# Kernel tuning notes

Hardware: AMD Instinct MI355X
Metric: run time of the kernel (lower is better)

## Reference

```python
import jax, jax.numpy as jnp
import numpy as np

N_EMBD = 2048
N_HEAD = 16
HEAD_SIZE = N_EMBD // N_HEAD


def setup_inputs() -> dict:
    key = jax.random.key(0)
    k1, k2, k3 = jax.random.split(key, 3)
    x = jax.random.normal(k1, (4, 2048, N_EMBD), dtype=jnp.float32)
    # Linear weights stored as (in, out) for x @ W
    scale = 1.0 / np.sqrt(N_EMBD)
    w_qkv = jax.random.normal(k2, (N_EMBD, 3 * N_EMBD), dtype=jnp.float32) * scale
    w_proj = jax.random.normal(k3, (N_EMBD, N_EMBD), dtype=jnp.float32) * scale
    return {"x": x, "w_qkv": w_qkv, "w_proj": w_proj}


def reference(x, w_qkv, w_proj):
    B, T, C = x.shape
    qkv = x @ w_qkv  # [B, T, 3C]
    q, k, v = jnp.split(qkv, 3, axis=-1)
    # [B, H, T, Dh]
    def heads(t):
        return t.reshape(B, T, N_HEAD, HEAD_SIZE).transpose(0, 2, 1, 3)
    q, k, v = heads(q), heads(k), heads(v)
    scores = jnp.einsum('bhqd,bhkd->bhqk', q, k) * (1.0 / np.sqrt(HEAD_SIZE))
    causal = jnp.tril(jnp.ones((T, T), dtype=bool))
    scores = jnp.where(causal, scores, jnp.finfo(scores.dtype).min)
    att = jax.nn.softmax(scores, axis=-1)
    y = jnp.einsum('bhqk,bhkd->bhqd', att, v)
    y = y.transpose(0, 2, 1, 3).reshape(B, T, C)
    return y @ w_proj
```

## Files before the change

kernel.cpp:

```cpp
#include <hip/hip_runtime.h>

typedef unsigned short u16;
typedef unsigned int u32;
typedef __bf16 bf16x8 __attribute__((ext_vector_type(8)));
typedef float f32x4 __attribute__((ext_vector_type(4)));

__device__ __forceinline__ u16 f2bf(float f) {
  u32 u = __builtin_bit_cast(u32, f);
  return (u16)((u + 0x7fffu + ((u >> 16) & 1u)) >> 16);
}

__device__ __forceinline__ f32x4 mfma16(bf16x8 a, bf16x8 b, f32x4 c) {
  return __builtin_amdgcn_mfma_f32_16x16x32_bf16(a, b, c, 0, 0, 0);
}

struct alignas(8) U16x4 { u16 x, y, z, w; };

#define AS1 __attribute__((address_space(1)))
#define AS3 __attribute__((address_space(3)))
__device__ __forceinline__ void gl16(const u16* g, u16* l) {
  __builtin_amdgcn_global_load_lds((const AS1 u32*)g, (AS3 u32*)l, 16, 0, 0);
}

__global__ __launch_bounds__(256) void k_f32_to_bf16(const float* __restrict__ in,
                                                     u16* __restrict__ out, long n4) {
  long i = (long)blockIdx.x * blockDim.x + threadIdx.x;
  long stride = (long)gridDim.x * blockDim.x;
  for (; i < n4; i += stride) {
    float4 v = ((const float4*)in)[i];
    U16x4 o{f2bf(v.x), f2bf(v.y), f2bf(v.z), f2bf(v.w)};
    ((U16x4*)out)[i] = o;
  }
}

__global__ __launch_bounds__(256) void k_transpose_f32_to_bf16(const float* __restrict__ in,
                                                               u16* __restrict__ out,
                                                               int rows, int cols) {
  __shared__ float tile[32][33];
  int bc = blockIdx.x * 32, br = blockIdx.y * 32;
  int tx = threadIdx.x, ty = threadIdx.y;
  for (int i = 0; i < 32; i += 8)
    tile[ty + i][tx] = in[(long)(br + ty + i) * cols + bc + tx];
  __syncthreads();
  for (int i = 0; i < 32; i += 8)
    out[(long)(bc + ty + i) * rows + br + tx] = f2bf(tile[tx][ty + i]);
}

__global__ __launch_bounds__(256) void k_transpose_v(const u16* __restrict__ qkv,
                                                     u16* __restrict__ vt) {
  __shared__ u16 tile[32][33];
  int bh = blockIdx.z; int b = bh >> 4, h = bh & 15;
  int t0 = blockIdx.y * 32, d0 = blockIdx.x * 32;
  int tx = threadIdx.x, ty = threadIdx.y;
  const u16* src = qkv + (long)(b * 2048) * 6144 + 4096 + h * 128;
  for (int i = 0; i < 32; i += 8)
    tile[ty + i][tx] = src[(long)(t0 + ty + i) * 6144 + d0 + tx];
  __syncthreads();
  u16* dst = vt + (long)bh * 128 * 2048;
  for (int i = 0; i < 32; i += 8)
    dst[(long)(d0 + ty + i) * 2048 + t0 + tx] = tile[tx][ty + i];
}

template <typename OutT>
__global__ __launch_bounds__(512, 2) void k_gemm256(const u16* __restrict__ A,
                                                    const u16* __restrict__ Bt,
                                                    OutT* __restrict__ C,
                                                    int M, int N, int K) {
  __shared__ alignas(16) u16 As[4][8192];
  __shared__ alignas(16) u16 Bs[4][8192];

  int gx = gridDim.x;
  int nwg = gx * gridDim.y;
  int bid = blockIdx.y * gx + blockIdx.x;
  int swz = (bid & 7) * (nwg >> 3) + (bid >> 3);
  int rem = swz % (gx * 4);
  int bx = rem >> 2;
  int by = (swz / (gx * 4)) * 4 + (rem & 3);

  int tid = threadIdx.x;
  int lane = tid & 63;
  int w = tid >> 6;
  int wr = w >> 2, wc = w & 3;
  int lr = lane & 15, lg = lane >> 4;
  long brow = (long)by * 256, bcol = (long)bx * 256;

  int rS[2], cS[2];
#pragma unroll
  for (int i = 0; i < 2; ++i) {
    int q = i * 512 + tid;
    rS[i] = q >> 2;
    cS[i] = ((q & 3) ^ ((rS[i] >> 1) & 3)) << 3;
  }
  const u16* Ab = A + brow * K;
  const u16* Bb = Bt + bcol * K;

  int offA[8], offB[4];
#pragma unroll
  for (int m = 0; m < 8; ++m) {
    int row = wr * 128 + m * 16 + lr;
    offA[m] = row * 32 + ((lg ^ ((row >> 1) & 3)) << 3);
  }
#pragma unroll
  for (int n = 0; n < 4; ++n) {
    int row = wc * 64 + n * 16 + lr;
    offB[n] = row * 32 + ((lg ^ ((row >> 1) & 3)) << 3);
  }

  f32x4 zero = {0.f, 0.f, 0.f, 0.f};
  f32x4 acc[8][4];
#pragma unroll
  for (int m = 0; m < 8; ++m)
#pragma unroll
    for (int n = 0; n < 4; ++n) acc[m][n] = zero;

  int NS = K >> 5;

#define STAGE256(SBUF, KT)                                                          \
  do {                                                                              \
    int kk_ = (KT) << 5;                                                            \
    gl16(Ab + (long)rS[0] * K + kk_ + cS[0], &As[SBUF][(0 * 512 + w * 64) * 8]);    \
    gl16(Ab + (long)rS[1] * K + kk_ + cS[1], &As[SBUF][(1 * 512 + w * 64) * 8]);    \
    gl16(Bb + (long)rS[0] * K + kk_ + cS[0], &Bs[SBUF][(0 * 512 + w * 64) * 8]);    \
    gl16(Bb + (long)rS[1] * K + kk_ + cS[1], &Bs[SBUF][(1 * 512 + w * 64) * 8]);    \
  } while (0)

  STAGE256(0, 0);
  STAGE256(1, 1);
  STAGE256(2, 2);
  asm volatile("s_waitcnt vmcnt(8)" ::: "memory");
  __builtin_amdgcn_s_barrier();

  for (int s = 0; s < NS; ++s) {
    int cb = s & 3;
    bf16x8 af[8], bfn[4];
#pragma unroll
    for (int m = 0; m < 8; ++m) af[m] = *(const bf16x8*)&As[cb][offA[m]];
#pragma unroll
    for (int n = 0; n < 4; ++n) bfn[n] = *(const bf16x8*)&Bs[cb][offB[n]];
    int t = s + 3;
    int tb = t & 3;
    if (t > NS - 1) t = NS - 1;
    STAGE256(tb, t);
    __builtin_amdgcn_s_setprio(1);
#pragma unroll
    for (int m = 0; m < 4; ++m)
#pragma unroll
      for (int n = 0; n < 4; ++n) acc[m][n] = mfma16(af[m], bfn[n], acc[m][n]);
    __builtin_amdgcn_s_setprio(0);
    __builtin_amdgcn_s_setprio(1);
#pragma unroll
    for (int m = 4; m < 8; ++m)
#pragma unroll
      for (int n = 0; n < 4; ++n) acc[m][n] = mfma16(af[m], bfn[n], acc[m][n]);
    __builtin_amdgcn_s_setprio(0);
    asm volatile("s_waitcnt vmcnt(8)" ::: "memory");
    __builtin_amdgcn_s_barrier();
  }
#undef STAGE256
  asm volatile("s_waitcnt vmcnt(0)" ::: "memory");

#pragma unroll
  for (int m = 0; m < 8; ++m)
#pragma unroll
    for (int n = 0; n < 4; ++n)
#pragma unroll
      for (int r = 0; r < 4; ++r) {
        long row = brow + wr * 128 + m * 16 + lg * 4 + r;
        long col = bcol + wc * 64 + n * 16 + lr;
        float v = acc[m][n][r];
        if constexpr (sizeof(OutT) == 2)
          C[row * N + col] = (OutT)f2bf(v);
        else
          C[row * N + col] = v;
      }
}

__global__ __launch_bounds__(256, 2) void k_attn2(const u16* __restrict__ qkv,
                                                  const u16* __restrict__ vt,
                                                  u16* __restrict__ y) {
  __shared__ alignas(16) u16 Ks[2][64 * 128];
  __shared__ alignas(16) u16 Vs[2][128 * 64];
  __shared__ alignas(16) u16 Ps[4][32 * 64];

  int bh = blockIdx.x;
  int qb = 15 - (int)blockIdx.y;
  int b = bh >> 4, h = bh & 15;
  int tid = threadIdx.x;
  int lane = tid & 63;
  int w = tid >> 6;
  int lr = lane & 15, lg = lane >> 4;
  int x7 = lr & 7;
  const float scale = 0.08838834764831845f;

  const u16* kbase = qkv + (long)(b * 2048) * 6144 + 2048 + h * 128;
  const u16* vtbh = vt + (long)bh * 128 * 2048;
  int qbase = qb * 128 + w * 32;

  const u16* qptr = qkv + (long)(qb * 128 + b * 2048) * 6144 + h * 128;
  bf16x8 qf[2][4];
  for (int qsub = 0; qsub < 2; ++qsub)
    for (int dc = 0; dc < 4; ++dc)
      qf[qsub][dc] = *(const bf16x8*)(qptr + (long)(w * 32 + qsub * 16 + lr) * 6144 + dc * 32 + lg * 8);

  f32x4 zero = {0.f, 0.f, 0.f, 0.f};
  f32x4 o[2][8];
  for (int qs = 0; qs < 2; ++qs)
    for (int ds = 0; ds < 8; ++ds) o[qs][ds] = zero;
  float m_run[2] = {-1e30f, -1e30f};
  float l_run[2] = {0.f, 0.f};

  int nkt = 2 * qb + 2;
  int qmaxw = qbase + 31;
  u16* Pw = &Ps[w][0];

#define STAGE(BUF, KT)                                                          \
  do {                                                                          \
    for (int i_ = 0; i_ < 4; ++i_) {                                            \
      int rl_ = w * 16 + i_ * 4;                                                \
      int row_ = rl_ + (lane >> 4);                                             \
      int ch_ = (lane & 15) ^ (row_ & 7);                                       \
      gl16(kbase + (long)((KT)*64 + row_) * 6144 + ch_ * 8, &Ks[BUF][rl_ * 128]); \
    }                                                                           \
    for (int i_ = 0; i_ < 4; ++i_) {                                            \
      int dl_ = w * 32 + i_ * 8;                                                \
      int d_ = dl_ + (lane >> 3);                                               \
      int ch_ = (lane & 7) ^ (d_ & 7);                                          \
      gl16(vtbh + (long)d_ * 2048 + (KT)*64 + ch_ * 8, &Vs[BUF][dl_ * 64]);     \
    }                                                                           \
  } while (0)

#define COMPUTE(BUF, KT)                                                        \
  do {                                                                          \
    const u16* Kb = &Ks[BUF][0];                                                \
    const u16* Vb = &Vs[BUF][0];                                                \
    f32x4 s[2][4];                                                              \
    for (int qs = 0; qs < 2; ++qs)                                              \
      for (int ks = 0; ks < 4; ++ks) s[qs][ks] = zero;                          \
    for (int ks = 0; ks < 4; ++ks) {                                            \
      int row = ks * 16 + lr;                                                   \
      for (int dc = 0; dc < 4; ++dc) {                                          \
        bf16x8 kf = *(const bf16x8*)(Kb + row * 128 + ((dc * 4 + lg) ^ x7) * 8); \
        s[0][ks] = mfma16(kf, qf[0][dc], s[0][ks]);                             \
        s[1][ks] = mfma16(kf, qf[1][dc], s[1][ks]);                             \
      }                                                                         \
    }                                                                           \
    for (int qs = 0; qs < 2; ++qs) {                                            \
      int qg = qbase + qs * 16 + lr;                                            \
      float p[16];                                                              \
      float tmax = -1e30f;                                                      \
      for (int ks = 0; ks < 4; ++ks)                                            \
        for (int r = 0; r < 4; ++r) {                                           \
          int key = (KT)*64 + ks * 16 + lg * 4 + r;                             \
          float v = (key <= qg) ? s[qs][ks][r] * scale : -1e30f;                \
          p[ks * 4 + r] = v;                                                    \
          tmax = fmaxf(tmax, v);                                                \
        }                                                                       \
      tmax = fmaxf(tmax, __shfl_xor(tmax, 16));                                 \
      tmax = fmaxf(tmax, __shfl_xor(tmax, 32));                                 \
      float m_new = fmaxf(m_run[qs], tmax);                                     \
      float alpha = __expf(m_run[qs] - m_new);                                  \
      float psum = 0.f;                                                         \
      for (int i = 0; i < 16; ++i) {                                            \
        p[i] = __expf(p[i] - m_new);                                            \
        psum += p[i];                                                           \
      }                                                                         \
      psum += __shfl_xor(psum, 16);                                             \
      psum += __shfl_xor(psum, 32);                                             \
      l_run[qs] = l_run[qs] * alpha + psum;                                     \
      m_run[qs] = m_new;                                                        \
      int prow = qs * 16 + lr;                                                  \
      for (int ks = 0; ks < 4; ++ks) {                                          \
        U16x4 pk{f2bf(p[ks * 4 + 0]), f2bf(p[ks * 4 + 1]),                      \
                 f2bf(p[ks * 4 + 2]), f2bf(p[ks * 4 + 3])};                     \
        int chunk = ks * 2 + (lg >> 1);                                         \
        *(U16x4*)&Pw[prow * 64 + ((chunk ^ x7) * 8) + (lg & 1) * 4] = pk;       \
      }                                                                         \
      float alr[4];                                                             \
      for (int r = 0; r < 4; ++r) alr[r] = __shfl(alpha, lg * 4 + r);           \
      for (int ds = 0; ds < 8; ++ds)                                            \
        for (int r = 0; r < 4; ++r) o[qs][ds][r] *= alr[r];                     \
    }                                                                           \
    asm volatile("s_waitcnt lgkmcnt(0)" ::: "memory");                          \
    for (int j = 0; j < 2; ++j) {                                               \
      int chv = ((j * 4 + lg) ^ x7) * 8;                                        \
      bf16x8 pa0 = *(const bf16x8*)&Pw[(0 * 16 + lr) * 64 + chv];               \
      bf16x8 pa1 = *(const bf16x8*)&Pw[(1 * 16 + lr) * 64 + chv];               \
      for (int ds = 0; ds < 8; ++ds) {                                          \
        bf16x8 vf = *(const bf16x8*)(Vb + (ds * 16 + lr) * 64 + chv);           \
        o[0][ds] = mfma16(pa0, vf, o[0][ds]);                                   \
        o[1][ds] = mfma16(pa1, vf, o[1][ds]);                                   \
      }                                                                         \
    }                                                                           \
  } while (0)

  int buf = 0;
  STAGE(0, 0);
  asm volatile("s_waitcnt vmcnt(0)" ::: "memory");
  __builtin_amdgcn_s_barrier();
  for (int kt = 0; kt < nkt - 1; ++kt) {
    STAGE(buf ^ 1, kt + 1);
    if (kt * 64 <= qmaxw) COMPUTE(buf, kt);
    asm volatile("s_waitcnt vmcnt(0) lgkmcnt(0)" ::: "memory");
    __builtin_amdgcn_s_barrier();
    buf ^= 1;
  }
  {
    int kt = nkt - 1;
    if (kt * 64 <= qmaxw) COMPUTE(buf, kt);
  }
#undef STAGE
#undef COMPUTE

  float linv[2][4];
  for (int qs = 0; qs < 2; ++qs)
    for (int r = 0; r < 4; ++r) linv[qs][r] = 1.0f / __shfl(l_run[qs], lg * 4 + r);
  u16* yb = y + (long)(b * 2048 + qb * 128 + w * 32) * 2048 + h * 128;
  for (int qs = 0; qs < 2; ++qs)
    for (int ds = 0; ds < 8; ++ds)
      for (int r = 0; r < 4; ++r)
        yb[(long)(qs * 16 + lg * 4 + r) * 2048 + ds * 16 + lr] = f2bf(o[qs][ds][r] * linv[qs][r]);
}

extern "C" void kernel_launch(void* const* d_in, const int* in_sizes, int n_in,
                              void* d_out, int out_size, void* d_ws, size_t ws_size,
                              hipStream_t stream) {
  const float* x = (const float*)d_in[0];
  const float* w_qkv = (const float*)d_in[1];
  const float* w_proj = (const float*)d_in[2];
  float* out = (float*)d_out;

  char* ws = (char*)d_ws;
  if (ws_size < 201326592ull) return;
  u16* QKV = (u16*)(ws);
  u16* WqT = (u16*)(ws + 100663296);
  u16* WpT = (u16*)(ws + 125829120);
  u16* Xb  = (u16*)(ws + 134217728);
  u16* Vt  = (u16*)(ws + 167772160);

  dim3 tb32x8(32, 8);

  k_f32_to_bf16<<<2048, 256, 0, stream>>>(x, Xb, (8192L * 2048) / 4);
  k_transpose_f32_to_bf16<<<dim3(192, 64), tb32x8, 0, stream>>>(w_qkv, WqT, 2048, 6144);
  k_transpose_f32_to_bf16<<<dim3(64, 64), tb32x8, 0, stream>>>(w_proj, WpT, 2048, 2048);

  k_gemm256<u16><<<dim3(24, 32), 512, 0, stream>>>(Xb, WqT, QKV, 8192, 6144, 2048);

  k_transpose_v<<<dim3(4, 64, 64), tb32x8, 0, stream>>>(QKV, Vt);

  k_attn2<<<dim3(64, 16), 256, 0, stream>>>(QKV, Vt, Xb );

  k_gemm256<float><<<dim3(8, 32), 512, 0, stream>>>(Xb, WpT, out, 8192, 2048, 2048);
}
```

Baseline: 416.9 us.

## Widen attention blocks to 256 queries with triple-buffered K/V pipeline

```diff
diff --git a/kernel.cpp b/kernel.cpp
--- a/kernel.cpp
+++ b/kernel.cpp
@@ -175,15 +175,16 @@
       }
 }
 
-__global__ __launch_bounds__(256, 2) void k_attn2(const u16* __restrict__ qkv,
+__global__ __launch_bounds__(512, 1) void k_attn3(const u16* __restrict__ qkv,
                                                   const u16* __restrict__ vt,
                                                   u16* __restrict__ y) {
-  __shared__ alignas(16) u16 Ks[2][64 * 128];
-  __shared__ alignas(16) u16 Vs[2][128 * 64];
-  __shared__ alignas(16) u16 Ps[4][32 * 64];
+  __shared__ alignas(16) u16 Ks[3][64 * 128];
+  __shared__ alignas(16) u16 Vs[3][128 * 64];
+  __shared__ alignas(16) u16 Ps[8][32 * 64];
 
   int bh = blockIdx.x;
-  int qb = 15 - (int)blockIdx.y;
+  int byy = blockIdx.y;
+  int qb = (byy < 4) ? (7 - byy) : (byy - 4);
   int b = bh >> 4, h = bh & 15;
   int tid = threadIdx.x;
   int lane = tid & 63;
@@ -194,35 +195,35 @@
 
   const u16* kbase = qkv + (long)(b * 2048) * 6144 + 2048 + h * 128;
   const u16* vtbh = vt + (long)bh * 128 * 2048;
-  int qbase = qb * 128 + w * 32;
-
-  const u16* qptr = qkv + (long)(qb * 128 + b * 2048) * 6144 + h * 128;
+  int qbase = qb * 256 + w * 32;
+  u16* Pw = &Ps[w][0];
+  f32x4 zero = {0.f, 0.f, 0.f, 0.f};
+
+  const u16* qptr = qkv + (long)(qb * 256 + b * 2048) * 6144 + h * 128;
   bf16x8 qf[2][4];
-  for (int qsub = 0; qsub < 2; ++qsub)
+  for (int qs = 0; qs < 2; ++qs)
     for (int dc = 0; dc < 4; ++dc)
-      qf[qsub][dc] = *(const bf16x8*)(qptr + (long)(w * 32 + qsub * 16 + lr) * 6144 + dc * 32 + lg * 8);
-
-  f32x4 zero = {0.f, 0.f, 0.f, 0.f};
+      qf[qs][dc] = *(const bf16x8*)(qptr + (long)(w * 32 + qs * 16 + lr) * 6144 + dc * 32 + lg * 8);
+
   f32x4 o[2][8];
   for (int qs = 0; qs < 2; ++qs)
     for (int ds = 0; ds < 8; ++ds) o[qs][ds] = zero;
   float m_run[2] = {-1e30f, -1e30f};
   float l_run[2] = {0.f, 0.f};
 
-  int nkt = 2 * qb + 2;
+  int nkt = 4 * qb + 4;
   int qmaxw = qbase + 31;
-  u16* Pw = &Ps[w][0];
 
 #define STAGE(BUF, KT)                                                          \
   do {                                                                          \
-    for (int i_ = 0; i_ < 4; ++i_) {                                            \
-      int rl_ = w * 16 + i_ * 4;                                                \
+    for (int i_ = 0; i_ < 2; ++i_) {                                            \
+      int rl_ = w * 8 + i_ * 4;                                                 \
       int row_ = rl_ + (lane >> 4);                                             \
       int ch_ = (lane & 15) ^ (row_ & 7);                                       \
       gl16(kbase + (long)((KT)*64 + row_) * 6144 + ch_ * 8, &Ks[BUF][rl_ * 128]); \
     }                                                                           \
-    for (int i_ = 0; i_ < 4; ++i_) {                                            \
-      int dl_ = w * 32 + i_ * 8;                                                \
+    for (int i_ = 0; i_ < 2; ++i_) {                                            \
+      int dl_ = w * 16 + i_ * 8;                                                \
       int d_ = dl_ + (lane >> 3);                                               \
       int ch_ = (lane & 7) ^ (d_ & 7);                                          \
       gl16(vtbh + (long)d_ * 2048 + (KT)*64 + ch_ * 8, &Vs[BUF][dl_ * 64]);     \
@@ -293,28 +294,28 @@
     }                                                                           \
   } while (0)
 
-  int buf = 0;
   STAGE(0, 0);
+  STAGE(1, 1);
+  asm volatile("s_waitcnt vmcnt(4)" ::: "memory");
+  __builtin_amdgcn_s_barrier();
+
+  int cbuf = 0, nbuf = 1, sbuf = 2;
+  for (int t = 0; t < nkt; ++t) {
+    int u = (t + 2 < nkt) ? t + 2 : nkt - 1;
+    STAGE(sbuf, u);
+    if (t * 64 <= qmaxw) COMPUTE(cbuf, t);
+    asm volatile("s_waitcnt vmcnt(4)" ::: "memory");
+    __builtin_amdgcn_s_barrier();
+    int tmp = cbuf; cbuf = nbuf; nbuf = sbuf; sbuf = tmp;
+  }
   asm volatile("s_waitcnt vmcnt(0)" ::: "memory");
-  __builtin_amdgcn_s_barrier();
-  for (int kt = 0; kt < nkt - 1; ++kt) {
-    STAGE(buf ^ 1, kt + 1);
-    if (kt * 64 <= qmaxw) COMPUTE(buf, kt);
-    asm volatile("s_waitcnt vmcnt(0) lgkmcnt(0)" ::: "memory");
-    __builtin_amdgcn_s_barrier();
-    buf ^= 1;
-  }
-  {
-    int kt = nkt - 1;
-    if (kt * 64 <= qmaxw) COMPUTE(buf, kt);
-  }
 #undef STAGE
 #undef COMPUTE
 
   float linv[2][4];
   for (int qs = 0; qs < 2; ++qs)
     for (int r = 0; r < 4; ++r) linv[qs][r] = 1.0f / __shfl(l_run[qs], lg * 4 + r);
-  u16* yb = y + (long)(b * 2048 + qb * 128 + w * 32) * 2048 + h * 128;
+  u16* yb = y + (long)(b * 2048 + qb * 256 + w * 32) * 2048 + h * 128;
   for (int qs = 0; qs < 2; ++qs)
     for (int ds = 0; ds < 8; ++ds)
       for (int r = 0; r < 4; ++r)
@@ -347,7 +348,7 @@
 
   k_transpose_v<<<dim3(4, 64, 64), tb32x8, 0, stream>>>(QKV, Vt);
 
-  k_attn2<<<dim3(64, 16), 256, 0, stream>>>(QKV, Vt, Xb );
+  k_attn3<<<dim3(64, 8), 512, 0, stream>>>(QKV, Vt, Xb );
 
   k_gemm256<float><<<dim3(8, 32), 512, 0, stream>>>(Xb, WpT, out, 8192, 2048, 2048);
 }
```

Result: slower. 439.9 us (+5.5%).
